# Kernel tuning notes

Hardware: AMD Instinct MI355X
Metric: run time of the kernel (lower is better)

The kernel has to match this reference:

```python
import jax, jax.numpy as jnp
import numpy as np

DIM = 128
SEQ = 8192

def setup_inputs() -> dict:
    key = jax.random.key(0)
    kq, kk, kv = jax.random.split(key, 3)
    Q = jax.random.normal(kq, (SEQ, DIM), dtype=jnp.float32)
    K = jax.random.normal(kk, (SEQ, DIM), dtype=jnp.float32)
    V = jax.random.normal(kv, (SEQ, DIM), dtype=jnp.float32)
    return {"Q": Q, "K": K, "V": V}

def reference(Q, K, V):
    # scores: [SEQ, SEQ]; scaled by sqrt(embedding dim) as in the torch module
    scale = 1.0 / np.sqrt(DIM).astype(np.float32)
    scores = jnp.einsum('qd,kd->qk', Q, K) * scale
    attn = jax.nn.softmax(scores, axis=-1)
    z = jnp.einsum('qk,kd->qd', attn, V)
    return z
```

## Files before the change

### kernel.cpp

```cpp
#include <hip/hip_runtime.h>
#include <hip/hip_bf16.h>

#define DIM 128
#define SEQ 8192
#define BRR 128
#define BC 64
#define NSPLIT 8
#define SPLITLEN (SEQ / NSPLIT)
#define QT2 (SEQ / BRR)
#define OP_ELEMS ((size_t)NSPLIT * SEQ * DIM)
#define L_ELEMS  ((size_t)NSPLIT * SEQ)
#define KST_OFF  (OP_ELEMS + L_ELEMS)
#define VST_OFF  (KST_OFF + (size_t)SEQ * DIM / 2)
#define WS_FLOATS (VST_OFF + (size_t)SEQ * DIM / 2)
#define SCALE_L2E 0.1275325340249306f

typedef __attribute__((ext_vector_type(8))) short short8;
typedef __attribute__((ext_vector_type(4))) float f32x4;
typedef __attribute__((ext_vector_type(16))) float f32x16;

__device__ __forceinline__ unsigned short f2bf(float f) {
  return __builtin_bit_cast(unsigned short, __float2bfloat16(f));
}
__device__ __forceinline__ unsigned int f2bf2(float a, float b) {
  return (unsigned int)f2bf(a) | ((unsigned int)f2bf(b) << 16);
}
__device__ __forceinline__ float fast_exp2(float x) {
#if __has_builtin(__builtin_amdgcn_exp2f)
  return __builtin_amdgcn_exp2f(x);
#else
  return exp2f(x);
#endif
}
__device__ __forceinline__ void async_cp16(const void* g, void* l) {
  __builtin_amdgcn_global_load_lds(
      (const __attribute__((address_space(1))) void*)g,
      (__attribute__((address_space(3))) void*)l, 16, 0, 0);
}

__global__ __launch_bounds__(256) void prep_kv(
    const float* __restrict__ K, const float* __restrict__ V,
    float* __restrict__ ws) {
  unsigned short* Kst = (unsigned short*)(ws + KST_OFF);
  unsigned short* Vst = (unsigned short*)(ws + VST_OFF);
  int cid = blockIdx.x * 256 + threadIdx.x;
  if (cid < 131072) {
    int n    = cid & 31;
    int hi   = (cid >> 5) & 1;
    int cc   = (cid >> 6) & 7;
    int kt2  = (cid >> 9) & 1;
    int tile = cid >> 10;
    int row  = tile * 64 + kt2 * 32 + n;
    const float* src = K + (size_t)row * DIM + cc * 16 + hi * 8;
    float4 a = *(const float4*)src;
    float4 b = *(const float4*)(src + 4);
    uint4 u;
    u.x = f2bf2(a.x, a.y); u.y = f2bf2(a.z, a.w);
    u.z = f2bf2(b.x, b.y); u.w = f2bf2(b.z, b.w);
    *(uint4*)&Kst[(size_t)cid * 8] = u;
  } else {
    int c    = cid - 131072;
    int n    = c & 31;
    int hi   = (c >> 5) & 1;
    int c2   = (c >> 6) & 3;
    int dt   = (c >> 8) & 3;
    int tile = c >> 10;
    const float* src = V + (size_t)(tile * 64 + c2 * 16 + hi * 8) * DIM + dt * 32 + n;
    float v[8];
    #pragma unroll
    for (int j = 0; j < 8; j++) v[j] = src[(size_t)j * DIM];
    uint4 u;
    u.x = f2bf2(v[0], v[1]); u.y = f2bf2(v[2], v[3]);
    u.z = f2bf2(v[4], v[5]); u.w = f2bf2(v[6], v[7]);
    *(uint4*)&Vst[(size_t)c * 8] = u;
  }
}

__global__ __launch_bounds__(256, 2) void attn_main(
    const float* __restrict__ Q, float* __restrict__ ws) {
  __shared__ __align__(16) unsigned short kt[64 * 128];
  __shared__ __align__(16) unsigned short vt[64 * 128];
  __shared__ __align__(16) unsigned short pt[4][32 * 72];

  const unsigned short* Kst = (const unsigned short*)(ws + KST_OFF);
  const unsigned short* Vst = (const unsigned short*)(ws + VST_OFF);

  const int tid  = threadIdx.x;
  const int wave = tid >> 6;
  const int lane = tid & 63;
  const int m    = lane & 31;
  const int hi   = lane >> 5;

  const int split = blockIdx.x;
  const int qtile = blockIdx.y;
  const int qbase = qtile * BRR + wave * 32;

  short8 qf[8];
  {
    const float* qrow = Q + (size_t)(qbase + m) * DIM + hi * 8;
    #pragma unroll
    for (int cc = 0; cc < 8; cc++) {
      float4 a = *(const float4*)(qrow + cc * 16);
      float4 b = *(const float4*)(qrow + cc * 16 + 4);
      short8 v;
      unsigned int u0 = f2bf2(a.x, a.y), u1 = f2bf2(a.z, a.w);
      unsigned int u2 = f2bf2(b.x, b.y), u3 = f2bf2(b.z, b.w);
      v[0] = (short)(u0 & 0xffff); v[1] = (short)(u0 >> 16);
      v[2] = (short)(u1 & 0xffff); v[3] = (short)(u1 >> 16);
      v[4] = (short)(u2 & 0xffff); v[5] = (short)(u2 >> 16);
      v[6] = (short)(u3 & 0xffff); v[7] = (short)(u3 >> 16);
      qf[cc] = v;
    }
  }

  float lsum[16];
  f32x16 accO[4];
  #pragma unroll
  for (int r = 0; r < 16; r++) lsum[r] = 0.f;
  #pragma unroll
  for (int dt = 0; dt < 4; dt++)
    #pragma unroll
    for (int r = 0; r < 16; r++) accO[dt][r] = 0.f;

  unsigned short* ptw = &pt[wave][0];

  const int tile0 = split * (SPLITLEN / 64);
  for (int it = 0; it < SPLITLEN / BC; it++) {
    const int tile = tile0 + it;
    __syncthreads();
    #pragma unroll
    for (int i = 0; i < 4; i++) {
      int ch = wave * 4 + i;
      async_cp16(Kst + (size_t)tile * 8192 + ch * 512 + lane * 8,
                 (char*)kt + ch * 1024);
      async_cp16(Vst + (size_t)tile * 8192 + ch * 512 + lane * 8,
                 (char*)vt + ch * 1024);
    }
    __syncthreads();

    f32x16 accS[2];
    #pragma unroll
    for (int kt2 = 0; kt2 < 2; kt2++) {
      f32x16 acc;
      #pragma unroll
      for (int r = 0; r < 16; r++) acc[r] = 0.f;
      #pragma unroll
      for (int cc = 0; cc < 8; cc++) {
        short8 b = *(const short8*)&kt[((kt2 * 8 + cc) * 64 + lane) * 8];
        acc = __builtin_amdgcn_mfma_f32_32x32x16_bf16(qf[cc], b, acc, 0, 0, 0);
      }
      accS[kt2] = acc;
    }

    #pragma unroll
    for (int kt2 = 0; kt2 < 2; kt2++) {
      #pragma unroll
      for (int reg = 0; reg < 16; reg++) {
        int row = (reg & 3) + 8 * (reg >> 2) + 4 * hi;
        float p = fast_exp2(accS[kt2][reg] * SCALE_L2E);
        lsum[reg] += p;
        ptw[row * 72 + kt2 * 32 + m] = f2bf(p);
      }
    }

    short8 ap[4];
    #pragma unroll
    for (int c2 = 0; c2 < 4; c2++)
      ap[c2] = *(const short8*)&ptw[m * 72 + c2 * 16 + hi * 8];

    #pragma unroll
    for (int dt = 0; dt < 4; dt++) {
      #pragma unroll
      for (int c2 = 0; c2 < 4; c2++) {
        short8 b = *(const short8*)&vt[((dt * 4 + c2) * 64 + lane) * 8];
        accO[dt] = __builtin_amdgcn_mfma_f32_32x32x16_bf16(ap[c2], b, accO[dt], 0, 0, 0);
      }
    }
  }

  #pragma unroll
  for (int reg = 0; reg < 16; reg++) {
    float l = lsum[reg];
    l += __shfl_xor(l, 1);
    l += __shfl_xor(l, 2);
    l += __shfl_xor(l, 4);
    l += __shfl_xor(l, 8);
    l += __shfl_xor(l, 16);
    lsum[reg] = l;
  }
  float* op = ws + (size_t)split * SEQ * DIM;
  float* lp = ws + OP_ELEMS + (size_t)split * SEQ;
  #pragma unroll
  for (int reg = 0; reg < 16; reg++) {
    int row  = (reg & 3) + 8 * (reg >> 2) + 4 * hi;
    int qrow = qbase + row;
    #pragma unroll
    for (int dt = 0; dt < 4; dt++)
      op[(size_t)qrow * DIM + dt * 32 + m] = accO[dt][reg];
    if (m == 0) lp[qrow] = lsum[reg];
  }
}

__global__ __launch_bounds__(256) void attn_combine(
    const float* __restrict__ ws, float* __restrict__ O) {
  int t = blockIdx.x * 256 + threadIdx.x;
  int qrow = t >> 5;
  int c4   = (t & 31) << 2;
  const float* lbase = ws + OP_ELEMS;
  float denom = 0.f;
  #pragma unroll
  for (int s = 0; s < NSPLIT; s++) denom += lbase[(size_t)s * SEQ + qrow];
  float4 acc = {0.f, 0.f, 0.f, 0.f};
  #pragma unroll
  for (int s = 0; s < NSPLIT; s++) {
    float4 v = *(const float4*)&ws[((size_t)s * SEQ + qrow) * DIM + c4];
    acc.x += v.x; acc.y += v.y; acc.z += v.z; acc.w += v.w;
  }
  float inv = 1.f / denom;
  float4 out = {acc.x * inv, acc.y * inv, acc.z * inv, acc.w * inv};
  *(float4*)&O[(size_t)qrow * DIM + c4] = out;
}

#define KSTR 136
#define VSTR 72
#define PSTR 72
__global__ __launch_bounds__(256, 1) void attn_fwd_fb(
    const float* __restrict__ Q, const float* __restrict__ K,
    const float* __restrict__ V, float* __restrict__ O) {
  __shared__ __align__(16) unsigned short kt[64 * KSTR];
  __shared__ __align__(16) unsigned short vt[DIM * VSTR];
  __shared__ __align__(16) unsigned short pt[4][16 * PSTR];
  const int tid = threadIdx.x, wave = tid >> 6, lane = tid & 63;
  const int l15 = lane & 15, quad = lane >> 4;
  const int qbase = blockIdx.x * 64 + wave * 16;
  short8 qf[4];
  {
    const float* qrow = Q + (size_t)(qbase + l15) * DIM + quad * 8;
    #pragma unroll
    for (int c = 0; c < 4; c++) {
      short8 v;
      #pragma unroll
      for (int j = 0; j < 8; j++) v[j] = (short)f2bf(qrow[c * 32 + j]);
      qf[c] = v;
    }
  }
  float lsum[4] = {0.f, 0.f, 0.f, 0.f};
  f32x4 o[8];
  const f32x4 fzero = {0.f, 0.f, 0.f, 0.f};
  #pragma unroll
  for (int d = 0; d < 8; d++) o[d] = fzero;
  unsigned short* pw = &pt[wave][0];
  for (int kv0 = 0; kv0 < SEQ; kv0 += 64) {
    __syncthreads();
    #pragma unroll
    for (int i = 0; i < 8; i++) {
      int idx = i * 256 + tid;
      int r = idx >> 5, c4 = (idx & 31) << 2;
      const float4 f = *(const float4*)(K + (size_t)(kv0 + r) * DIM + c4);
      uint2 u = {f2bf2(f.x, f.y), f2bf2(f.z, f.w)};
      *(uint2*)&kt[r * KSTR + c4] = u;
    }
    #pragma unroll
    for (int i = 0; i < 8; i++) {
      int idx = i * 256 + tid;
      int c = idx & 127, g = idx >> 7;
      const float* src = V + (size_t)(kv0 + 4 * g) * DIM + c;
      uint2 u = {f2bf2(src[0], src[DIM]), f2bf2(src[2 * DIM], src[3 * DIM])};
      *(uint2*)&vt[c * VSTR + 4 * g] = u;
    }
    __syncthreads();
    f32x4 s[4];
    #pragma unroll
    for (int blk = 0; blk < 4; blk++) {
      f32x4 acc = fzero;
      const unsigned short* kr = &kt[(blk * 16 + l15) * KSTR + quad * 8];
      #pragma unroll
      for (int c = 0; c < 4; c++)
        acc = __builtin_amdgcn_mfma_f32_16x16x32_bf16(qf[c], *(const short8*)&kr[c * 32], acc, 0, 0, 0);
      s[blk] = acc;
    }
    #pragma unroll
    for (int r = 0; r < 4; r++) {
      #pragma unroll
      for (int blk = 0; blk < 4; blk++) {
        float p = fast_exp2(s[blk][r] * SCALE_L2E);
        lsum[r] += p;
        pw[(quad * 4 + r) * PSTR + blk * 16 + l15] = f2bf(p);
      }
    }
    short8 ap0 = *(const short8*)&pw[l15 * PSTR + quad * 8];
    short8 ap1 = *(const short8*)&pw[l15 * PSTR + 32 + quad * 8];
    #pragma unroll
    for (int d = 0; d < 8; d++) {
      const unsigned short* vr = &vt[(d * 16 + l15) * VSTR + quad * 8];
      o[d] = __builtin_amdgcn_mfma_f32_16x16x32_bf16(ap0, *(const short8*)&vr[0], o[d], 0, 0, 0);
      o[d] = __builtin_amdgcn_mfma_f32_16x16x32_bf16(ap1, *(const short8*)&vr[32], o[d], 0, 0, 0);
    }
  }
  #pragma unroll
  for (int r = 0; r < 4; r++) {
    float l = lsum[r];
    l += __shfl_xor(l, 1); l += __shfl_xor(l, 2);
    l += __shfl_xor(l, 4); l += __shfl_xor(l, 8);
    float inv = 1.f / l;
    float* orow = O + (size_t)(qbase + quad * 4 + r) * DIM + l15;
    #pragma unroll
    for (int d = 0; d < 8; d++) orow[d * 16] = o[d][r] * inv;
  }
}

extern "C" void kernel_launch(void* const* d_in, const int* in_sizes, int n_in,
                              void* d_out, int out_size, void* d_ws, size_t ws_size,
                              hipStream_t stream) {
  const float* Q = (const float*)d_in[0];
  const float* K = (const float*)d_in[1];
  const float* V = (const float*)d_in[2];
  float* O = (float*)d_out;
  const size_t need = WS_FLOATS * sizeof(float);
  if (ws_size >= need) {
    float* ws = (float*)d_ws;
    hipLaunchKernelGGL(prep_kv, dim3(1024), dim3(256), 0, stream, K, V, ws);
    hipLaunchKernelGGL(attn_main, dim3(NSPLIT, QT2), dim3(256), 0, stream, Q, ws);
    hipLaunchKernelGGL(attn_combine, dim3(1024), dim3(256), 0, stream, ws, O);
  } else {
    hipLaunchKernelGGL(attn_fwd_fb, dim3(SEQ / 64), dim3(256), 0, stream, Q, K, V, O);
  }
}
```

Baseline: 116.9 us.

## Read K fragments directly from global and stage K prep through swizzled LDS

The K-side of prep_kv now runs 32 rows per block: it loads rows with coalesced float4 reads, converts them to bf16, writes them into an XOR-swizzled LDS tile, then writes out the MFMA-fragment layout, using fewer blocks. In attn_main the K tile is no longer copied into LDS; each wave reads its B fragments straight from the pre-laid-out global buffer, which frees LDS and drops half the async copies. The cost is that every wave now fetches K from global/L2 on its own, where before the block shared one LDS copy, so each K tile is read four times and the loads sit right before the MFMAs.

```diff
diff --git a/kernel.cpp b/kernel.cpp
--- a/kernel.cpp
+++ b/kernel.cpp
@@ -43,23 +43,34 @@
     float* __restrict__ ws) {
   unsigned short* Kst = (unsigned short*)(ws + KST_OFF);
   unsigned short* Vst = (unsigned short*)(ws + VST_OFF);
-  int cid = blockIdx.x * 256 + threadIdx.x;
-  if (cid < 131072) {
-    int n    = cid & 31;
-    int hi   = (cid >> 5) & 1;
-    int cc   = (cid >> 6) & 7;
-    int kt2  = (cid >> 9) & 1;
-    int tile = cid >> 10;
-    int row  = tile * 64 + kt2 * 32 + n;
-    const float* src = K + (size_t)row * DIM + cc * 16 + hi * 8;
-    float4 a = *(const float4*)src;
-    float4 b = *(const float4*)(src + 4);
-    uint4 u;
-    u.x = f2bf2(a.x, a.y); u.y = f2bf2(a.z, a.w);
-    u.z = f2bf2(b.x, b.y); u.w = f2bf2(b.z, b.w);
-    *(uint4*)&Kst[(size_t)cid * 8] = u;
+  const int t = threadIdx.x;
+  if (blockIdx.x < 256) {
+    __shared__ __align__(16) unsigned short klds[32 * 128];
+    const int r0 = blockIdx.x * 32;
+    #pragma unroll
+    for (int i = 0; i < 4; i++) {
+      int idx = i * 256 + t;
+      int r  = idx >> 5;
+      int c4 = (idx & 31) << 2;
+      int g  = c4 >> 3;
+      const float4 f = *(const float4*)(K + (size_t)(r0 + r) * DIM + c4);
+      uint2 u = {f2bf2(f.x, f.y), f2bf2(f.z, f.w)};
+      *(uint2*)&klds[r * 128 + ((g ^ (r & 7)) << 3) + (c4 & 7)] = u;
+    }
+    __syncthreads();
+    const size_t base = (size_t)blockIdx.x * 512;
+    #pragma unroll
+    for (int e = 0; e < 2; e++) {
+      int c  = e * 256 + t;
+      int n  = c & 31;
+      int hi = (c >> 5) & 1;
+      int cc = c >> 6;
+      int g  = cc * 2 + hi;
+      uint4 u = *(const uint4*)&klds[n * 128 + ((g ^ (n & 7)) << 3)];
+      *(uint4*)&Kst[(base + (size_t)g * 32 + n) * 8] = u;
+    }
   } else {
-    int c    = cid - 131072;
+    int c    = (blockIdx.x - 256) * 256 + t;
     int n    = c & 31;
     int hi   = (c >> 5) & 1;
     int c2   = (c >> 6) & 3;
@@ -78,7 +89,6 @@
 
 __global__ __launch_bounds__(256, 2) void attn_main(
     const float* __restrict__ Q, float* __restrict__ ws) {
-  __shared__ __align__(16) unsigned short kt[64 * 128];
   __shared__ __align__(16) unsigned short vt[64 * 128];
   __shared__ __align__(16) unsigned short pt[4][32 * 72];
 
@@ -131,13 +141,12 @@
     #pragma unroll
     for (int i = 0; i < 4; i++) {
       int ch = wave * 4 + i;
-      async_cp16(Kst + (size_t)tile * 8192 + ch * 512 + lane * 8,
-                 (char*)kt + ch * 1024);
       async_cp16(Vst + (size_t)tile * 8192 + ch * 512 + lane * 8,
                  (char*)vt + ch * 1024);
     }
     __syncthreads();
 
+    const unsigned short* ktile = Kst + (size_t)tile * 8192;
     f32x16 accS[2];
     #pragma unroll
     for (int kt2 = 0; kt2 < 2; kt2++) {
@@ -146,7 +155,7 @@
       for (int r = 0; r < 16; r++) acc[r] = 0.f;
       #pragma unroll
       for (int cc = 0; cc < 8; cc++) {
-        short8 b = *(const short8*)&kt[((kt2 * 8 + cc) * 64 + lane) * 8];
+        short8 b = *(const short8*)&ktile[((kt2 * 8 + cc) * 64 + lane) * 8];
         acc = __builtin_amdgcn_mfma_f32_32x32x16_bf16(qf[cc], b, acc, 0, 0, 0);
       }
       accS[kt2] = acc;
@@ -319,7 +328,7 @@
   const size_t need = WS_FLOATS * sizeof(float);
   if (ws_size >= need) {
     float* ws = (float*)d_ws;
-    hipLaunchKernelGGL(prep_kv, dim3(1024), dim3(256), 0, stream, K, V, ws);
+    hipLaunchKernelGGL(prep_kv, dim3(768), dim3(256), 0, stream, K, V, ws);
     hipLaunchKernelGGL(attn_main, dim3(NSPLIT, QT2), dim3(256), 0, stream, Q, ws);
     hipLaunchKernelGGL(attn_combine, dim3(1024), dim3(256), 0, stream, ws, O);
   } else {
```

Result: slower. 162.5 us (+39.1%).
